# Kernel tuning notes

Measured on AMD Instinct MI355X. Metric: run time of the kernel, lower is better.

The kernel has to match this reference:

```python
import jax, jax.numpy as jnp
import numpy as np

N_NODES = 100000
N_EDGES = 1600000
D_IN = 128
HID = 128
E_CH = 16


def setup_inputs() -> dict:
    key = jax.random.key(0)
    ks = jax.random.split(key, 16)

    def glorot(k, shape):
        fan_in, fan_out = shape[0], shape[1]
        lim = jnp.sqrt(6.0 / (fan_in + fan_out))
        return jax.random.uniform(k, shape, jnp.float32, -lim, lim)

    inp = {
        "x": jax.random.normal(ks[0], (N_NODES, D_IN), jnp.float32),
        "edge_index": jax.random.randint(ks[1], (2, N_EDGES), 0, N_NODES, jnp.int32),
        "edge_attr": jax.random.normal(ks[2], (N_EDGES, E_CH), jnp.float32),
        # SAGEConv layer 0: lin_l (neighbor agg, with bias), lin_r (root, no bias)
        "Wl0": glorot(ks[3], (D_IN, HID)),
        "Wr0": glorot(ks[4], (D_IN, HID)),
        "b0": jnp.zeros((HID,), jnp.float32),
        # SAGEConv layer 1
        "Wl1": glorot(ks[5], (HID, HID)),
        "Wr1": glorot(ks[6], (HID, HID)),
        "b1": jnp.zeros((HID,), jnp.float32),
        # classifier MLP: (2*HID + E_CH) -> 128 -> 64 -> 1
        "Wc1": glorot(ks[7], (2 * HID + E_CH, 128)),
        "bc1": jnp.zeros((128,), jnp.float32),
        "Wc2": glorot(ks[8], (128, 64)),
        "bc2": jnp.zeros((64,), jnp.float32),
        "Wc3": glorot(ks[9], (64, 1)),
        "bc3": jnp.zeros((1,), jnp.float32),
    }
    return inp


def _sage_conv(x, src, dst, Wl, Wr, b):
    # PyG SAGEConv (aggr='mean'): out = lin_l(mean_j x_j) + lin_r(x_i)
    # messages flow src -> dst
    msg_sum = jax.ops.segment_sum(x[src], dst, num_segments=N_NODES)  # [N, D]
    deg = jax.ops.segment_sum(jnp.ones((src.shape[0],), x.dtype), dst,
                              num_segments=N_NODES)                   # [N]
    agg = msg_sum / jnp.maximum(deg, 1.0)[:, None]  # mean; isolated nodes -> 0
    return agg @ Wl + b + x @ Wr


def reference(x, edge_index, edge_attr,
              Wl0, Wr0, b0, Wl1, Wr1, b1,
              Wc1, bc1, Wc2, bc2, Wc3, bc3):
    src, dst = edge_index[0], edge_index[1]
    # encode: two SAGEConv layers, each followed by ReLU (dropout is identity at eval)
    h = jax.nn.relu(_sage_conv(x, src, dst, Wl0, Wr0, b0))
    h = jax.nn.relu(_sage_conv(h, src, dst, Wl1, Wr1, b1))
    # edge classifier: gather endpoint embeddings, concat edge features
    feat = jnp.concatenate([h[src], h[dst], edge_attr], axis=-1)  # [E, 2H+EC]
    z = jax.nn.relu(feat @ Wc1 + bc1)
    z = jax.nn.relu(z @ Wc2 + bc2)
    logits = (z @ Wc3 + bc3).reshape(-1)  # [E]
    return jax.nn.sigmoid(logits)
```

## Files before the change

kernel.cpp:

```cpp
#include <hip/hip_runtime.h>
#include <hip/hip_bf16.h>
#include <math.h>

#define NN 100000
#define NE 1600000
#define NBLK 391
#define ZS 296

typedef __bf16 bf16x8 __attribute__((ext_vector_type(8)));
typedef float f32x4 __attribute__((ext_vector_type(4)));

union BF8 { bf16x8 v; unsigned short u[8]; };

static __device__ __forceinline__ unsigned short f2bf(float f) {
  unsigned int u = __float_as_uint(f);
  unsigned int r = u + 0x7fffu + ((u >> 16) & 1u);
  return (unsigned short)(r >> 16);
}
static __device__ __forceinline__ float bf2f(unsigned short b) {
  return __uint_as_float((unsigned int)b << 16);
}
static __device__ __forceinline__ f32x4 zero4() {
  f32x4 z = {0.f, 0.f, 0.f, 0.f}; return z;
}
static __device__ __forceinline__ bf16x8 zerobf8() {
  BF8 t;
  #pragma unroll
  for (int j = 0; j < 8; ++j) t.u[j] = 0;
  return t.v;
}
static __device__ __forceinline__ bf16x8 cvt8(float4 v0, float4 v1, float s) {
  BF8 t;
  t.u[0]=f2bf(v0.x*s); t.u[1]=f2bf(v0.y*s); t.u[2]=f2bf(v0.z*s); t.u[3]=f2bf(v0.w*s);
  t.u[4]=f2bf(v1.x*s); t.u[5]=f2bf(v1.y*s); t.u[6]=f2bf(v1.z*s); t.u[7]=f2bf(v1.w*s);
  return t.v;
}

__global__ void prep_swizzle(const float* __restrict__ Wl0, const float* __restrict__ Wr0,
                             const float* __restrict__ Wl1, const float* __restrict__ Wr1,
                             const float* __restrict__ Wc1, const float* __restrict__ Wc2,
                             __hip_bfloat16* __restrict__ swz) {
  int gid = blockIdx.x * 256 + threadIdx.x;
  if (gid >= 110592) return;
  int id = gid;
  const float* A; const float* B = nullptr; int KC, Nc, Ksrc;
  if (id < 32768)        { KC = 8; Nc = 128; Ksrc = 256; A = Wl0; B = Wr0; }
  else if (id < 65536)   { id -= 32768; KC = 8; Nc = 128; Ksrc = 256; A = Wl1; B = Wr1; }
  else if (id < 81920)   { id -= 65536; KC = 4; Nc = 128; Ksrc = 128; A = Wc1; }
  else if (id < 98304)   { id -= 81920; KC = 4; Nc = 128; Ksrc = 128; A = Wc1 + 128 * 128; }
  else if (id < 102400)  { id -= 98304; KC = 1; Nc = 128; Ksrc = 16;  A = Wc1 + 256 * 128; }
  else                   { id -= 102400; KC = 4; Nc = 64;  Ksrc = 128; A = Wc2; }
  int j = id & 7, lane = (id >> 3) & 63, rest = id >> 9;
  int c = rest % KC, t = rest / KC;
  int k = c * 32 + (lane >> 4) * 8 + j;
  int n = t * 16 + (lane & 15);
  float v = 0.f;
  if (k < Ksrc) {
    if (B && k >= 128) v = B[(k - 128) * Nc + n];
    else               v = A[k * Nc + n];
  }
  unsigned short* o = (unsigned short*)swz;
  o[gid] = f2bf(v);
}

__global__ void x_to_bf16(const float* __restrict__ x, __hip_bfloat16* __restrict__ xb) {
  int i = blockIdx.x * 256 + threadIdx.x;
  float4 v = ((const float4*)x)[i];
  ushort4 p;
  p.x = f2bf(v.x); p.y = f2bf(v.y); p.z = f2bf(v.z); p.w = f2bf(v.w);
  ((ushort4*)xb)[i] = p;
}

__global__ void deg_count(const int* __restrict__ ei, int* __restrict__ degCnt) {
  int e = blockIdx.x * 256 + threadIdx.x;
  atomicAdd(&degCnt[ei[NE + e]], 1);
}

__global__ void scan_block_sums(const int* __restrict__ degCnt, int* __restrict__ blockSums) {
  __shared__ int red[4];
  int i = blockIdx.x * 256 + threadIdx.x;
  int v = (i < NN) ? degCnt[i] : 0;
  #pragma unroll
  for (int off = 32; off; off >>= 1) v += __shfl_down(v, off, 64);
  if ((threadIdx.x & 63) == 0) red[threadIdx.x >> 6] = v;
  __syncthreads();
  if (threadIdx.x == 0) blockSums[blockIdx.x] = red[0] + red[1] + red[2] + red[3];
}

__global__ void scan_partials(const int* __restrict__ blockSums, int* __restrict__ blockOff) {
  __shared__ int lds[512];
  int t = threadIdx.x;
  int v = (t < NBLK) ? blockSums[t] : 0;
  lds[t] = v; __syncthreads();
  #pragma unroll
  for (int off = 1; off < 512; off <<= 1) {
    int a = (t >= off) ? lds[t - off] : 0;
    __syncthreads();
    lds[t] += a;
    __syncthreads();
  }
  if (t < NBLK) blockOff[t] = lds[t] - v;
}

__global__ void scan_write(const int* __restrict__ degCnt, const int* __restrict__ blockOff,
                           int* __restrict__ rowPtr, int* __restrict__ cursor) {
  __shared__ int lds[256];
  int t = threadIdx.x;
  int i = blockIdx.x * 256 + t;
  int v = (i < NN) ? degCnt[i] : 0;
  lds[t] = v; __syncthreads();
  #pragma unroll
  for (int off = 1; off < 256; off <<= 1) {
    int a = (t >= off) ? lds[t - off] : 0;
    __syncthreads();
    lds[t] += a;
    __syncthreads();
  }
  if (i < NN) {
    int excl = blockOff[blockIdx.x] + lds[t] - v;
    rowPtr[i] = excl;
    cursor[i] = excl;
  }
}

__global__ void csr_fill(const int* __restrict__ ei, int* __restrict__ cursor,
                         int* __restrict__ csrSrc, int2* __restrict__ csrDE) {
  int e = blockIdx.x * 256 + threadIdx.x;
  int s = ei[e], d = ei[NE + e];
  int idx = atomicAdd(&cursor[d], 1);
  csrSrc[idx] = s;
  csrDE[idx] = make_int2(d, e);
}

__global__ __launch_bounds__(256, 8)
void gather_agg(const __hip_bfloat16* __restrict__ xb,
                const int* __restrict__ csrSrc, const int* __restrict__ rowPtr,
                const int* __restrict__ degCnt, __hip_bfloat16* __restrict__ msgOut) {
  int g = threadIdx.x >> 4, c16 = threadIdx.x & 15;
  int n = blockIdx.x * 16 + g;
  int rp = rowPtr[n], dg = degCnt[n];
  float a[8];
  #pragma unroll
  for (int j = 0; j < 8; ++j) a[j] = 0.f;
  for (int i = 0; i < dg; i += 4) {
    #pragma unroll
    for (int k = 0; k < 4; ++k) {
      int ii = i + k;
      int s = csrSrc[rp + (ii < dg ? ii : dg - 1)];
      uint4 u = *(const uint4*)((const unsigned short*)xb + (size_t)s * 128 + c16 * 8);
      if (ii < dg) {
        a[0] += bf2f((unsigned short)(u.x & 0xffff)); a[1] += bf2f((unsigned short)(u.x >> 16));
        a[2] += bf2f((unsigned short)(u.y & 0xffff)); a[3] += bf2f((unsigned short)(u.y >> 16));
        a[4] += bf2f((unsigned short)(u.z & 0xffff)); a[5] += bf2f((unsigned short)(u.z >> 16));
        a[6] += bf2f((unsigned short)(u.w & 0xffff)); a[7] += bf2f((unsigned short)(u.w >> 16));
      }
    }
  }
  float r = 1.f / fmaxf((float)dg, 1.f);
  uint4 p;
  p.x = (unsigned)f2bf(a[0] * r) | ((unsigned)f2bf(a[1] * r) << 16);
  p.y = (unsigned)f2bf(a[2] * r) | ((unsigned)f2bf(a[3] * r) << 16);
  p.z = (unsigned)f2bf(a[4] * r) | ((unsigned)f2bf(a[5] * r) << 16);
  p.w = (unsigned)f2bf(a[6] * r) | ((unsigned)f2bf(a[7] * r) << 16);
  *(uint4*)((unsigned short*)msgOut + (size_t)n * 128 + c16 * 8) = p;
}

__global__ __launch_bounds__(256, 2)
void node_gemm(const __hip_bfloat16* __restrict__ msgB,
               const __hip_bfloat16* __restrict__ selfB16,
               const __hip_bfloat16* __restrict__ swzW, const float* __restrict__ bias,
               __hip_bfloat16* __restrict__ hOut) {
  const int tid = threadIdx.x, w = tid >> 6, lane = tid & 63;
  const int l15 = lane & 15, quad = lane >> 4;
  const int nBase = blockIdx.x * 256 + w * 64;

  int row[4];
  #pragma unroll
  for (int t = 0; t < 4; ++t) {
    int n = nBase + t * 16 + l15;
    if (n > NN - 1) n = NN - 1;
    row[t] = n;
  }

  f32x4 acc[8][4];
  #pragma unroll
  for (int mt = 0; mt < 8; ++mt)
    #pragma unroll
    for (int nt = 0; nt < 4; ++nt) acc[mt][nt] = zero4();

  #pragma unroll
  for (int c = 0; c < 8; ++c) {
    bf16x8 bfr[4];
    if (c < 4) {
      #pragma unroll
      for (int nt = 0; nt < 4; ++nt)
        bfr[nt] = *(const bf16x8*)(msgB + (size_t)row[nt] * 128 + c * 32 + quad * 8);
    } else {
      #pragma unroll
      for (int nt = 0; nt < 4; ++nt)
        bfr[nt] = *(const bf16x8*)(selfB16 + (size_t)row[nt] * 128 + (c - 4) * 32 + quad * 8);
    }
    bf16x8 afr[8];
    #pragma unroll
    for (int mt = 0; mt < 8; ++mt)
      afr[mt] = *(const bf16x8*)(swzW + ((mt * 8 + c) * 64 + lane) * 8);
    #pragma unroll
    for (int mt = 0; mt < 8; ++mt)
      #pragma unroll
      for (int nt = 0; nt < 4; ++nt)
        acc[mt][nt] = __builtin_amdgcn_mfma_f32_16x16x32_bf16(afr[mt], bfr[nt], acc[mt][nt], 0, 0, 0);
  }

  #pragma unroll
  for (int mt = 0; mt < 8; ++mt) {
    const float4 b4 = *(const float4*)(bias + mt * 16 + quad * 4);
    #pragma unroll
    for (int nt = 0; nt < 4; ++nt) {
      int n = nBase + nt * 16 + l15;
      if (n < NN) {
        ushort4 p;
        p.x = f2bf(fmaxf(acc[mt][nt][0] + b4.x, 0.f));
        p.y = f2bf(fmaxf(acc[mt][nt][1] + b4.y, 0.f));
        p.z = f2bf(fmaxf(acc[mt][nt][2] + b4.z, 0.f));
        p.w = f2bf(fmaxf(acc[mt][nt][3] + b4.w, 0.f));
        *(ushort4*)(hOut + (size_t)n * 128 + mt * 16 + quad * 4) = p;
      }
    }
  }
}

__global__ __launch_bounds__(256, 2)
void pq_gemm(const __hip_bfloat16* __restrict__ h1, const __hip_bfloat16* __restrict__ swzPQ,
             __hip_bfloat16* __restrict__ Pout, __hip_bfloat16* __restrict__ Qout) {
  const __hip_bfloat16* swzW = swzPQ + blockIdx.y * 16384;
  __hip_bfloat16* outp = blockIdx.y ? Qout : Pout;
  const int tid = threadIdx.x, w = tid >> 6, lane = tid & 63;
  const int l15 = lane & 15, quad = lane >> 4;
  const int nBase = blockIdx.x * 256 + w * 64;

  int row[4];
  #pragma unroll
  for (int t = 0; t < 4; ++t) {
    int n = nBase + t * 16 + l15;
    if (n > NN - 1) n = NN - 1;
    row[t] = n;
  }

  f32x4 acc[8][4];
  #pragma unroll
  for (int mt = 0; mt < 8; ++mt)
    #pragma unroll
    for (int nt = 0; nt < 4; ++nt) acc[mt][nt] = zero4();

  #pragma unroll
  for (int c = 0; c < 4; ++c) {
    bf16x8 bfr[4];
    #pragma unroll
    for (int nt = 0; nt < 4; ++nt)
      bfr[nt] = *(const bf16x8*)(h1 + (size_t)row[nt] * 128 + c * 32 + quad * 8);
    bf16x8 afr[8];
    #pragma unroll
    for (int mt = 0; mt < 8; ++mt)
      afr[mt] = *(const bf16x8*)(swzW + ((mt * 4 + c) * 64 + lane) * 8);
    #pragma unroll
    for (int mt = 0; mt < 8; ++mt)
      #pragma unroll
      for (int nt = 0; nt < 4; ++nt)
        acc[mt][nt] = __builtin_amdgcn_mfma_f32_16x16x32_bf16(afr[mt], bfr[nt], acc[mt][nt], 0, 0, 0);
  }

  #pragma unroll
  for (int mt = 0; mt < 8; ++mt) {
    #pragma unroll
    for (int nt = 0; nt < 4; ++nt) {
      int n = nBase + nt * 16 + l15;
      if (n < NN) {
        ushort4 p;
        p.x = f2bf(acc[mt][nt][0]);
        p.y = f2bf(acc[mt][nt][1]);
        p.z = f2bf(acc[mt][nt][2]);
        p.w = f2bf(acc[mt][nt][3]);
        *(ushort4*)(outp + (size_t)n * 128 + mt * 16 + quad * 4) = p;
      }
    }
  }
}

__global__ __launch_bounds__(256, 4)
void edge_mlp(const __hip_bfloat16* __restrict__ P, const __hip_bfloat16* __restrict__ Q,
              const float* __restrict__ ea,
              const int* __restrict__ csrSrc, const int2* __restrict__ csrDE,
              const __hip_bfloat16* __restrict__ swzWea, const __hip_bfloat16* __restrict__ swzWc2,
              const float* __restrict__ Wc3, const float* __restrict__ bc1,
              const float* __restrict__ bc2, const float* __restrict__ bc3,
              float* __restrict__ out) {
  __shared__ char lds[4 * 32 * ZS];
  const int tid = threadIdx.x, w = tid >> 6, lane = tid & 63;
  const int l15 = lane & 15, quad = lane >> 4;
  const int eBase = blockIdx.x * 128 + w * 32;
  char* zbuf = lds + w * (32 * ZS);

  int srcO[2], dstO[2], eid[2];
  #pragma unroll
  for (int t = 0; t < 2; ++t) {
    int p = eBase + t * 16 + l15;
    srcO[t] = csrSrc[p] * 128;
    int2 de = csrDE[p];
    dstO[t] = de.x * 128;
    eid[t] = de.y;
  }

  ushort4 pA[2][4];
  #pragma unroll
  for (int nt = 0; nt < 2; ++nt)
    #pragma unroll
    for (int mt = 0; mt < 4; ++mt)
      pA[nt][mt] = *(const ushort4*)(P + srcO[nt] + mt * 16 + quad * 4);

  bf16x8 bfr[2];
  #pragma unroll
  for (int nt = 0; nt < 2; ++nt) {
    if (quad < 2) {
      const float4* pe = (const float4*)(ea + (size_t)eid[nt] * 16 + quad * 8);
      bfr[nt] = cvt8(pe[0], pe[1], 1.f);
    } else {
      bfr[nt] = zerobf8();
    }
  }

  f32x4 acc[4][2];
  #pragma unroll
  for (int mt = 0; mt < 4; ++mt)
    #pragma unroll
    for (int nt = 0; nt < 2; ++nt) acc[mt][nt] = zero4();
  #pragma unroll
  for (int mt = 0; mt < 4; ++mt) {
    bf16x8 afr = *(const bf16x8*)(swzWea + (mt * 64 + lane) * 8);
    #pragma unroll
    for (int nt = 0; nt < 2; ++nt)
      acc[mt][nt] = __builtin_amdgcn_mfma_f32_16x16x32_bf16(afr, bfr[nt], acc[mt][nt], 0, 0, 0);
  }

  ushort4 pB[2][4], qA[2][4];
  #pragma unroll
  for (int nt = 0; nt < 2; ++nt)
    #pragma unroll
    for (int mt = 0; mt < 4; ++mt)
      pB[nt][mt] = *(const ushort4*)(P + srcO[nt] + (mt + 4) * 16 + quad * 4);
  #pragma unroll
  for (int nt = 0; nt < 2; ++nt)
    #pragma unroll
    for (int mt = 0; mt < 4; ++mt)
      qA[nt][mt] = *(const ushort4*)(Q + dstO[nt] + mt * 16 + quad * 4);

  #pragma unroll
  for (int mt = 0; mt < 4; ++mt) {
    const int cb = mt * 16 + quad * 4;
    const float4 b4 = *(const float4*)(bc1 + cb);
    #pragma unroll
    for (int nt = 0; nt < 2; ++nt) {
      ushort4 pu = pA[nt][mt];
      ushort4 qu = qA[nt][mt];
      int er = nt * 16 + l15;
      ushort4 z;
      z.x = f2bf(fmaxf(acc[mt][nt][0] + bf2f(pu.x) + bf2f(qu.x) + b4.x, 0.f));
      z.y = f2bf(fmaxf(acc[mt][nt][1] + bf2f(pu.y) + bf2f(qu.y) + b4.y, 0.f));
      z.z = f2bf(fmaxf(acc[mt][nt][2] + bf2f(pu.z) + bf2f(qu.z) + b4.z, 0.f));
      z.w = f2bf(fmaxf(acc[mt][nt][3] + bf2f(pu.w) + bf2f(qu.w) + b4.w, 0.f));
      *(ushort4*)(zbuf + er * ZS + cb * 2) = z;
    }
  }

  #pragma unroll
  for (int mt = 0; mt < 4; ++mt)
    #pragma unroll
    for (int nt = 0; nt < 2; ++nt) acc[mt][nt] = zero4();
  #pragma unroll
  for (int mt = 0; mt < 4; ++mt) {
    bf16x8 afr = *(const bf16x8*)(swzWea + ((mt + 4) * 64 + lane) * 8);
    #pragma unroll
    for (int nt = 0; nt < 2; ++nt)
      acc[mt][nt] = __builtin_amdgcn_mfma_f32_16x16x32_bf16(afr, bfr[nt], acc[mt][nt], 0, 0, 0);
  }

  ushort4 qB[2][4];
  #pragma unroll
  for (int nt = 0; nt < 2; ++nt)
    #pragma unroll
    for (int mt = 0; mt < 4; ++mt)
      qB[nt][mt] = *(const ushort4*)(Q + dstO[nt] + (mt + 4) * 16 + quad * 4);

  #pragma unroll
  for (int mt = 0; mt < 4; ++mt) {
    const int cb = (mt + 4) * 16 + quad * 4;
    const float4 b4 = *(const float4*)(bc1 + cb);
    #pragma unroll
    for (int nt = 0; nt < 2; ++nt) {
      ushort4 pu = pB[nt][mt];
      ushort4 qu = qB[nt][mt];
      int er = nt * 16 + l15;
      ushort4 z;
      z.x = f2bf(fmaxf(acc[mt][nt][0] + bf2f(pu.x) + bf2f(qu.x) + b4.x, 0.f));
      z.y = f2bf(fmaxf(acc[mt][nt][1] + bf2f(pu.y) + bf2f(qu.y) + b4.y, 0.f));
      z.z = f2bf(fmaxf(acc[mt][nt][2] + bf2f(pu.z) + bf2f(qu.z) + b4.z, 0.f));
      z.w = f2bf(fmaxf(acc[mt][nt][3] + bf2f(pu.w) + bf2f(qu.w) + b4.w, 0.f));
      *(ushort4*)(zbuf + er * ZS + cb * 2) = z;
    }
  }

  f32x4 acc2[4][2];
  #pragma unroll
  for (int mt = 0; mt < 4; ++mt)
    #pragma unroll
    for (int nt = 0; nt < 2; ++nt) acc2[mt][nt] = zero4();

  #pragma unroll
  for (int c = 0; c < 4; ++c) {
    bf16x8 b2[2];
    #pragma unroll
    for (int nt = 0; nt < 2; ++nt)
      b2[nt] = *(const bf16x8*)(zbuf + (nt * 16 + l15) * ZS + (c * 32 + quad * 8) * 2);
    #pragma unroll
    for (int mt = 0; mt < 4; ++mt) {
      bf16x8 afr = *(const bf16x8*)(swzWc2 + ((mt * 4 + c) * 64 + lane) * 8);
      #pragma unroll
      for (int nt = 0; nt < 2; ++nt)
        acc2[mt][nt] = __builtin_amdgcn_mfma_f32_16x16x32_bf16(afr, b2[nt], acc2[mt][nt], 0, 0, 0);
    }
  }

  #pragma unroll
  for (int mt = 0; mt < 4; ++mt) {
    const int cb = mt * 16 + quad * 4;
    const float4 b4 = *(const float4*)(bc2 + cb);
    #pragma unroll
    for (int nt = 0; nt < 2; ++nt) {
      int er = nt * 16 + l15;
      ushort4 z;
      z.x = f2bf(fmaxf(acc2[mt][nt][0] + b4.x, 0.f));
      z.y = f2bf(fmaxf(acc2[mt][nt][1] + b4.y, 0.f));
      z.z = f2bf(fmaxf(acc2[mt][nt][2] + b4.z, 0.f));
      z.w = f2bf(fmaxf(acc2[mt][nt][3] + b4.w, 0.f));
      *(ushort4*)(zbuf + er * ZS + cb * 2) = z;
    }
  }

  {
    int e = lane & 31, half = lane >> 5;
    float a3 = (half == 0) ? bc3[0] : 0.f;
    #pragma unroll
    for (int k2 = 0; k2 < 16; ++k2) {
      unsigned int u = *(const unsigned int*)(zbuf + e * ZS + half * 64 + k2 * 4);
      float v0 = __uint_as_float(u << 16);
      float v1 = __uint_as_float(u & 0xffff0000u);
      const float2 wv = *(const float2*)(Wc3 + half * 32 + 2 * k2);
      a3 += v0 * wv.x + v1 * wv.y;
    }
    a3 += __shfl_xor(a3, 32);
    if (half == 0) {
      int oe = csrDE[eBase + e].y;
      out[oe] = 1.f / (1.f + __expf(-a3));
    }
  }
}

extern "C" void kernel_launch(void* const* d_in, const int* in_sizes, int n_in,
                              void* d_out, int out_size, void* d_ws, size_t ws_size,
                              hipStream_t stream) {
  const float* x   = (const float*)d_in[0];
  const int*   ei  = (const int*)d_in[1];
  const float* ea  = (const float*)d_in[2];
  const float* Wl0 = (const float*)d_in[3];
  const float* Wr0 = (const float*)d_in[4];
  const float* b0  = (const float*)d_in[5];
  const float* Wl1 = (const float*)d_in[6];
  const float* Wr1 = (const float*)d_in[7];
  const float* b1  = (const float*)d_in[8];
  const float* Wc1 = (const float*)d_in[9];
  const float* bc1 = (const float*)d_in[10];
  const float* Wc2 = (const float*)d_in[11];
  const float* bc2 = (const float*)d_in[12];
  const float* Wc3 = (const float*)d_in[13];
  const float* bc3 = (const float*)d_in[14];
  float* out = (float*)d_out;

  char* ws = (char*)d_ws;
  int* degCnt    = (int*)(ws + 0);
  int* rowPtr    = (int*)(ws + 400000);
  int* cursor    = (int*)(ws + 800000);
  int* blockSums = (int*)(ws + 1200000);
  int* blockOff  = (int*)(ws + 1202048);
  int* csrSrc    = (int*)(ws + 1204096);
  int2* csrDE    = (int2*)(ws + 7604096);
  __hip_bfloat16* bufB = (__hip_bfloat16*)(ws + 20404096);
  __hip_bfloat16* bufC = (__hip_bfloat16*)(ws + 46004096);
  __hip_bfloat16* bufD = (__hip_bfloat16*)(ws + 71604096);
  __hip_bfloat16* swz  = (__hip_bfloat16*)(ws + 97204096);
  __hip_bfloat16* msgB = bufB; __hip_bfloat16* Pb = bufB;
  __hip_bfloat16* h0b  = bufC; __hip_bfloat16* Qb = bufC;
  __hip_bfloat16* xb   = bufD; __hip_bfloat16* h1b = bufD;

  hipMemsetAsync(degCnt, 0, 400000, stream);
  prep_swizzle<<<432, 256, 0, stream>>>(Wl0, Wr0, Wl1, Wr1, Wc1, Wc2, swz);
  x_to_bf16<<<12500, 256, 0, stream>>>(x, xb);

  deg_count<<<NE / 256, 256, 0, stream>>>(ei, degCnt);
  scan_block_sums<<<NBLK, 256, 0, stream>>>(degCnt, blockSums);
  scan_partials<<<1, 512, 0, stream>>>(blockSums, blockOff);
  scan_write<<<NBLK, 256, 0, stream>>>(degCnt, blockOff, rowPtr, cursor);
  csr_fill<<<NE / 256, 256, 0, stream>>>(ei, cursor, csrSrc, csrDE);

  gather_agg<<<NN / 16, 256, 0, stream>>>(xb, csrSrc, rowPtr, degCnt, msgB);
  node_gemm<<<NBLK, 256, 0, stream>>>(msgB, xb, swz, b0, h0b);

  gather_agg<<<NN / 16, 256, 0, stream>>>(h0b, csrSrc, rowPtr, degCnt, msgB);
  node_gemm<<<NBLK, 256, 0, stream>>>(msgB, h0b, swz + 32768, b1, h1b);

  pq_gemm<<<dim3(NBLK, 2), 256, 0, stream>>>(h1b, swz + 65536, Pb, Qb);
  edge_mlp<<<NE / 128, 256, 0, stream>>>(Pb, Qb, ea, csrSrc, csrDE,
                                         swz + 98304, swz + 102400,
                                         Wc3, bc1, bc2, bc3, out);
}
```

Baseline: 845.9 us.

## Fuse neighbor gather, SAGE node GEMM and P/Q projection into one kernel

Replaces the separate gather_agg, node_gemm and pq_gemm launches with a single fused_sage kernel per layer. Each block aggregates 64 nodes into LDS, then runs the node GEMM from LDS; on the second layer h1 stays in LDS and feeds the P/Q projection directly. This removes the global round trips for the mean-aggregated messages and for h1, plus three launches. In exchange each block handles fewer nodes, the weight fragments are re-read by many more blocks, and occupancy is tied to the 34 KB of LDS per block.

```diff
diff --git a/kernel.cpp b/kernel.cpp
--- a/kernel.cpp
+++ b/kernel.cpp
@@ -6,6 +6,7 @@
 #define NE 1600000
 #define NBLK 391
 #define ZS 296
+#define RS 272
 
 typedef __bf16 bf16x8 __attribute__((ext_vector_type(8)));
 typedef float f32x4 __attribute__((ext_vector_type(4)));
@@ -132,155 +133,159 @@
   csrDE[idx] = make_int2(d, e);
 }
 
-__global__ __launch_bounds__(256, 8)
-void gather_agg(const __hip_bfloat16* __restrict__ xb,
+__global__ __launch_bounds__(256, 4)
+void fused_sage(const __hip_bfloat16* __restrict__ feat,
                 const int* __restrict__ csrSrc, const int* __restrict__ rowPtr,
-                const int* __restrict__ degCnt, __hip_bfloat16* __restrict__ msgOut) {
-  int g = threadIdx.x >> 4, c16 = threadIdx.x & 15;
-  int n = blockIdx.x * 16 + g;
-  int rp = rowPtr[n], dg = degCnt[n];
-  float a[8];
-  #pragma unroll
-  for (int j = 0; j < 8; ++j) a[j] = 0.f;
-  for (int i = 0; i < dg; i += 4) {
-    #pragma unroll
-    for (int k = 0; k < 4; ++k) {
-      int ii = i + k;
-      int s = csrSrc[rp + (ii < dg ? ii : dg - 1)];
-      uint4 u = *(const uint4*)((const unsigned short*)xb + (size_t)s * 128 + c16 * 8);
-      if (ii < dg) {
-        a[0] += bf2f((unsigned short)(u.x & 0xffff)); a[1] += bf2f((unsigned short)(u.x >> 16));
-        a[2] += bf2f((unsigned short)(u.y & 0xffff)); a[3] += bf2f((unsigned short)(u.y >> 16));
-        a[4] += bf2f((unsigned short)(u.z & 0xffff)); a[5] += bf2f((unsigned short)(u.z >> 16));
-        a[6] += bf2f((unsigned short)(u.w & 0xffff)); a[7] += bf2f((unsigned short)(u.w >> 16));
+                const int* __restrict__ degCnt,
+                const __hip_bfloat16* __restrict__ swzW, const float* __restrict__ bias,
+                __hip_bfloat16* __restrict__ hOut,
+                int doPQ, const __hip_bfloat16* __restrict__ swzPQ,
+                __hip_bfloat16* __restrict__ Pout, __hip_bfloat16* __restrict__ Qout) {
+  __shared__ __align__(16) char msgL[64 * RS];
+  __shared__ __align__(16) char hL[64 * RS];
+  const int tid = threadIdx.x;
+  const int nBase = blockIdx.x * 64;
+
+  {
+    int g = tid >> 4, c16 = tid & 15;
+    for (int r = 0; r < 4; ++r) {
+      int nl = r * 16 + g;
+      int n = nBase + nl;
+      float a[8];
+      #pragma unroll
+      for (int j = 0; j < 8; ++j) a[j] = 0.f;
+      float rinv = 0.f;
+      if (n < NN) {
+        int rp = rowPtr[n], dg = degCnt[n];
+        for (int i = 0; i < dg; i += 4) {
+          #pragma unroll
+          for (int k = 0; k < 4; ++k) {
+            int ii = i + k;
+            int s = csrSrc[rp + (ii < dg ? ii : dg - 1)];
+            uint4 u = *(const uint4*)((const unsigned short*)feat + (size_t)s * 128 + c16 * 8);
+            if (ii < dg) {
+              a[0] += bf2f((unsigned short)(u.x & 0xffff)); a[1] += bf2f((unsigned short)(u.x >> 16));
+              a[2] += bf2f((unsigned short)(u.y & 0xffff)); a[3] += bf2f((unsigned short)(u.y >> 16));
+              a[4] += bf2f((unsigned short)(u.z & 0xffff)); a[5] += bf2f((unsigned short)(u.z >> 16));
+              a[6] += bf2f((unsigned short)(u.w & 0xffff)); a[7] += bf2f((unsigned short)(u.w >> 16));
+            }
+          }
+        }
+        rinv = 1.f / fmaxf((float)dg, 1.f);
       }
-    }
-  }
-  float r = 1.f / fmaxf((float)dg, 1.f);
-  uint4 p;
-  p.x = (unsigned)f2bf(a[0] * r) | ((unsigned)f2bf(a[1] * r) << 16);
-  p.y = (unsigned)f2bf(a[2] * r) | ((unsigned)f2bf(a[3] * r) << 16);
-  p.z = (unsigned)f2bf(a[4] * r) | ((unsigned)f2bf(a[5] * r) << 16);
-  p.w = (unsigned)f2bf(a[6] * r) | ((unsigned)f2bf(a[7] * r) << 16);
-  *(uint4*)((unsigned short*)msgOut + (size_t)n * 128 + c16 * 8) = p;
-}
-
-__global__ __launch_bounds__(256, 2)
-void node_gemm(const __hip_bfloat16* __restrict__ msgB,
-               const __hip_bfloat16* __restrict__ selfB16,
-               const __hip_bfloat16* __restrict__ swzW, const float* __restrict__ bias,
-               __hip_bfloat16* __restrict__ hOut) {
-  const int tid = threadIdx.x, w = tid >> 6, lane = tid & 63;
+      uint4 p;
+      p.x = (unsigned)f2bf(a[0] * rinv) | ((unsigned)f2bf(a[1] * rinv) << 16);
+      p.y = (unsigned)f2bf(a[2] * rinv) | ((unsigned)f2bf(a[3] * rinv) << 16);
+      p.z = (unsigned)f2bf(a[4] * rinv) | ((unsigned)f2bf(a[5] * rinv) << 16);
+      p.w = (unsigned)f2bf(a[6] * rinv) | ((unsigned)f2bf(a[7] * rinv) << 16);
+      *(uint4*)(msgL + nl * RS + c16 * 16) = p;
+    }
+  }
+  __syncthreads();
+
+  const int w = tid >> 6, lane = tid & 63;
   const int l15 = lane & 15, quad = lane >> 4;
-  const int nBase = blockIdx.x * 256 + w * 64;
-
-  int row[4];
-  #pragma unroll
-  for (int t = 0; t < 4; ++t) {
-    int n = nBase + t * 16 + l15;
-    if (n > NN - 1) n = NN - 1;
-    row[t] = n;
-  }
-
-  f32x4 acc[8][4];
-  #pragma unroll
-  for (int mt = 0; mt < 8; ++mt)
-    #pragma unroll
-    for (int nt = 0; nt < 4; ++nt) acc[mt][nt] = zero4();
-
-  #pragma unroll
-  for (int c = 0; c < 8; ++c) {
-    bf16x8 bfr[4];
-    if (c < 4) {
+  int rowg[4];
+  #pragma unroll
+  for (int nt = 0; nt < 4; ++nt) {
+    int n = nBase + nt * 16 + l15;
+    rowg[nt] = (n < NN) ? n : (NN - 1);
+  }
+
+  {
+    f32x4 acc[2][4];
+    #pragma unroll
+    for (int mi = 0; mi < 2; ++mi)
+      #pragma unroll
+      for (int nt = 0; nt < 4; ++nt) acc[mi][nt] = zero4();
+
+    #pragma unroll
+    for (int c = 0; c < 8; ++c) {
+      bf16x8 bfr[4];
+      if (c < 4) {
+        #pragma unroll
+        for (int nt = 0; nt < 4; ++nt)
+          bfr[nt] = *(const bf16x8*)(msgL + (nt * 16 + l15) * RS + (c * 32 + quad * 8) * 2);
+      } else {
+        #pragma unroll
+        for (int nt = 0; nt < 4; ++nt)
+          bfr[nt] = *(const bf16x8*)(feat + (size_t)rowg[nt] * 128 + (c - 4) * 32 + quad * 8);
+      }
+      #pragma unroll
+      for (int mi = 0; mi < 2; ++mi) {
+        int mt = w * 2 + mi;
+        bf16x8 afr = *(const bf16x8*)(swzW + ((mt * 8 + c) * 64 + lane) * 8);
+        #pragma unroll
+        for (int nt = 0; nt < 4; ++nt)
+          acc[mi][nt] = __builtin_amdgcn_mfma_f32_16x16x32_bf16(afr, bfr[nt], acc[mi][nt], 0, 0, 0);
+      }
+    }
+
+    #pragma unroll
+    for (int mi = 0; mi < 2; ++mi) {
+      int mt = w * 2 + mi;
+      const int cb = mt * 16 + quad * 4;
+      const float4 b4 = *(const float4*)(bias + cb);
+      #pragma unroll
+      for (int nt = 0; nt < 4; ++nt) {
+        ushort4 p;
+        p.x = f2bf(fmaxf(acc[mi][nt][0] + b4.x, 0.f));
+        p.y = f2bf(fmaxf(acc[mi][nt][1] + b4.y, 0.f));
+        p.z = f2bf(fmaxf(acc[mi][nt][2] + b4.z, 0.f));
+        p.w = f2bf(fmaxf(acc[mi][nt][3] + b4.w, 0.f));
+        if (doPQ) {
+          *(ushort4*)(hL + (nt * 16 + l15) * RS + cb * 2) = p;
+        } else {
+          int n = nBase + nt * 16 + l15;
+          if (n < NN)
+            *(ushort4*)(hOut + (size_t)n * 128 + cb) = p;
+        }
+      }
+    }
+  }
+
+  if (doPQ) {
+    __syncthreads();
+    f32x4 acc2[4][4];
+    #pragma unroll
+    for (int mi = 0; mi < 4; ++mi)
+      #pragma unroll
+      for (int nt = 0; nt < 4; ++nt) acc2[mi][nt] = zero4();
+
+    #pragma unroll
+    for (int c = 0; c < 4; ++c) {
+      bf16x8 bfr[4];
       #pragma unroll
       for (int nt = 0; nt < 4; ++nt)
-        bfr[nt] = *(const bf16x8*)(msgB + (size_t)row[nt] * 128 + c * 32 + quad * 8);
-    } else {
-      #pragma unroll
-      for (int nt = 0; nt < 4; ++nt)
-        bfr[nt] = *(const bf16x8*)(selfB16 + (size_t)row[nt] * 128 + (c - 4) * 32 + quad * 8);
-    }
-    bf16x8 afr[8];
-    #pragma unroll
-    for (int mt = 0; mt < 8; ++mt)
-      afr[mt] = *(const bf16x8*)(swzW + ((mt * 8 + c) * 64 + lane) * 8);
-    #pragma unroll
-    for (int mt = 0; mt < 8; ++mt)
-      #pragma unroll
-      for (int nt = 0; nt < 4; ++nt)
-        acc[mt][nt] = __builtin_amdgcn_mfma_f32_16x16x32_bf16(afr[mt], bfr[nt], acc[mt][nt], 0, 0, 0);
-  }
-
-  #pragma unroll
-  for (int mt = 0; mt < 8; ++mt) {
-    const float4 b4 = *(const float4*)(bias + mt * 16 + quad * 4);
-    #pragma unroll
-    for (int nt = 0; nt < 4; ++nt) {
-      int n = nBase + nt * 16 + l15;
-      if (n < NN) {
-        ushort4 p;
-        p.x = f2bf(fmaxf(acc[mt][nt][0] + b4.x, 0.f));
-        p.y = f2bf(fmaxf(acc[mt][nt][1] + b4.y, 0.f));
-        p.z = f2bf(fmaxf(acc[mt][nt][2] + b4.z, 0.f));
-        p.w = f2bf(fmaxf(acc[mt][nt][3] + b4.w, 0.f));
-        *(ushort4*)(hOut + (size_t)n * 128 + mt * 16 + quad * 4) = p;
+        bfr[nt] = *(const bf16x8*)(hL + (nt * 16 + l15) * RS + (c * 32 + quad * 8) * 2);
+      #pragma unroll
+      for (int mi = 0; mi < 4; ++mi) {
+        int mtg = w * 4 + mi;
+        const __hip_bfloat16* base = swzPQ + ((mtg < 8) ? 0 : 16384);
+        int t = mtg & 7;
+        bf16x8 afr = *(const bf16x8*)(base + ((t * 4 + c) * 64 + lane) * 8);
+        #pragma unroll
+        for (int nt = 0; nt < 4; ++nt)
+          acc2[mi][nt] = __builtin_amdgcn_mfma_f32_16x16x32_bf16(afr, bfr[nt], acc2[mi][nt], 0, 0, 0);
       }
     }
-  }
-}
-
-__global__ __launch_bounds__(256, 2)
-void pq_gemm(const __hip_bfloat16* __restrict__ h1, const __hip_bfloat16* __restrict__ swzPQ,
-             __hip_bfloat16* __restrict__ Pout, __hip_bfloat16* __restrict__ Qout) {
-  const __hip_bfloat16* swzW = swzPQ + blockIdx.y * 16384;
-  __hip_bfloat16* outp = blockIdx.y ? Qout : Pout;
-  const int tid = threadIdx.x, w = tid >> 6, lane = tid & 63;
-  const int l15 = lane & 15, quad = lane >> 4;
-  const int nBase = blockIdx.x * 256 + w * 64;
-
-  int row[4];
-  #pragma unroll
-  for (int t = 0; t < 4; ++t) {
-    int n = nBase + t * 16 + l15;
-    if (n > NN - 1) n = NN - 1;
-    row[t] = n;
-  }
-
-  f32x4 acc[8][4];
-  #pragma unroll
-  for (int mt = 0; mt < 8; ++mt)
-    #pragma unroll
-    for (int nt = 0; nt < 4; ++nt) acc[mt][nt] = zero4();
-
-  #pragma unroll
-  for (int c = 0; c < 4; ++c) {
-    bf16x8 bfr[4];
-    #pragma unroll
-    for (int nt = 0; nt < 4; ++nt)
-      bfr[nt] = *(const bf16x8*)(h1 + (size_t)row[nt] * 128 + c * 32 + quad * 8);
-    bf16x8 afr[8];
-    #pragma unroll
-    for (int mt = 0; mt < 8; ++mt)
-      afr[mt] = *(const bf16x8*)(swzW + ((mt * 4 + c) * 64 + lane) * 8);
-    #pragma unroll
-    for (int mt = 0; mt < 8; ++mt)
-      #pragma unroll
-      for (int nt = 0; nt < 4; ++nt)
-        acc[mt][nt] = __builtin_amdgcn_mfma_f32_16x16x32_bf16(afr[mt], bfr[nt], acc[mt][nt], 0, 0, 0);
-  }
-
-  #pragma unroll
-  for (int mt = 0; mt < 8; ++mt) {
-    #pragma unroll
-    for (int nt = 0; nt < 4; ++nt) {
-      int n = nBase + nt * 16 + l15;
-      if (n < NN) {
-        ushort4 p;
-        p.x = f2bf(acc[mt][nt][0]);
-        p.y = f2bf(acc[mt][nt][1]);
-        p.z = f2bf(acc[mt][nt][2]);
-        p.w = f2bf(acc[mt][nt][3]);
-        *(ushort4*)(outp + (size_t)n * 128 + mt * 16 + quad * 4) = p;
+
+    #pragma unroll
+    for (int mi = 0; mi < 4; ++mi) {
+      int mtg = w * 4 + mi;
+      __hip_bfloat16* outp = (mtg < 8) ? Pout : Qout;
+      const int cb = (mtg & 7) * 16 + quad * 4;
+      #pragma unroll
+      for (int nt = 0; nt < 4; ++nt) {
+        int n = nBase + nt * 16 + l15;
+        if (n < NN) {
+          ushort4 p;
+          p.x = f2bf(acc2[mi][nt][0]);
+          p.y = f2bf(acc2[mi][nt][1]);
+          p.z = f2bf(acc2[mi][nt][2]);
+          p.w = f2bf(acc2[mi][nt][3]);
+          *(ushort4*)(outp + (size_t)n * 128 + cb) = p;
+        }
       }
     }
   }
@@ -496,9 +501,10 @@
   __hip_bfloat16* bufC = (__hip_bfloat16*)(ws + 46004096);
   __hip_bfloat16* bufD = (__hip_bfloat16*)(ws + 71604096);
   __hip_bfloat16* swz  = (__hip_bfloat16*)(ws + 97204096);
-  __hip_bfloat16* msgB = bufB; __hip_bfloat16* Pb = bufB;
-  __hip_bfloat16* h0b  = bufC; __hip_bfloat16* Qb = bufC;
-  __hip_bfloat16* xb   = bufD; __hip_bfloat16* h1b = bufD;
+  __hip_bfloat16* Pb  = bufB;
+  __hip_bfloat16* h0b = bufC;
+  __hip_bfloat16* xb  = bufD;
+  __hip_bfloat16* Qb  = bufD;
 
   hipMemsetAsync(degCnt, 0, 400000, stream);
   prep_swizzle<<<432, 256, 0, stream>>>(Wl0, Wr0, Wl1, Wr1, Wc1, Wc2, swz);
@@ -510,13 +516,11 @@
   scan_write<<<NBLK, 256, 0, stream>>>(degCnt, blockOff, rowPtr, cursor);
   csr_fill<<<NE / 256, 256, 0, stream>>>(ei, cursor, csrSrc, csrDE);
 
-  gather_agg<<<NN / 16, 256, 0, stream>>>(xb, csrSrc, rowPtr, degCnt, msgB);
-  node_gemm<<<NBLK, 256, 0, stream>>>(msgB, xb, swz, b0, h0b);
-
-  gather_agg<<<NN / 16, 256, 0, stream>>>(h0b, csrSrc, rowPtr, degCnt, msgB);
-  node_gemm<<<NBLK, 256, 0, stream>>>(msgB, h0b, swz + 32768, b1, h1b);
-
-  pq_gemm<<<dim3(NBLK, 2), 256, 0, stream>>>(h1b, swz + 65536, Pb, Qb);
+  fused_sage<<<1563, 256, 0, stream>>>(xb, csrSrc, rowPtr, degCnt, swz, b0, h0b,
+                                       0, nullptr, nullptr, nullptr);
+  fused_sage<<<1563, 256, 0, stream>>>(h0b, csrSrc, rowPtr, degCnt, swz + 32768, b1, nullptr,
+                                       1, swz + 65536, Pb, Qb);
+
   edge_mlp<<<NE / 128, 256, 0, stream>>>(Pb, Qb, ea, csrSrc, csrDE,
                                          swz + 98304, swz + 102400,
                                          Wc3, bc1, bc2, bc3, out);
```

New measurement: 897.2 us. 6.1% more time.

## Fuse layer-1 SAGE GEMM with P/Q projection via LDS-resident h1

Applied to the files above, without the earlier changes.

The second node_gemm and the pq_gemm kernel are merged into one kernel. Each warp writes its bias+ReLU h1 tile to LDS and immediately runs both P and Q projections from it. This removes the global write and re-read of h1 and one kernel launch. In exchange, each block uses about 75 KB of LDS, the P/Q work runs on half as many blocks, and buffers are re-aliased so P overwrites msgB in place.

```diff
diff --git a/kernel.cpp b/kernel.cpp
--- a/kernel.cpp
+++ b/kernel.cpp
@@ -230,13 +230,16 @@
 }
 
 __global__ __launch_bounds__(256, 2)
-void pq_gemm(const __hip_bfloat16* __restrict__ h1, const __hip_bfloat16* __restrict__ swzPQ,
-             __hip_bfloat16* __restrict__ Pout, __hip_bfloat16* __restrict__ Qout) {
-  const __hip_bfloat16* swzW = swzPQ + blockIdx.y * 16384;
-  __hip_bfloat16* outp = blockIdx.y ? Qout : Pout;
+void node_pq_gemm(const __hip_bfloat16* __restrict__ msgB,
+                  const __hip_bfloat16* __restrict__ selfB16,
+                  const __hip_bfloat16* __restrict__ swzW, const float* __restrict__ bias,
+                  const __hip_bfloat16* __restrict__ swzPQ,
+                  __hip_bfloat16* __restrict__ Pout, __hip_bfloat16* __restrict__ Qout) {
+  __shared__ __align__(16) char hLds[4 * 64 * ZS];
   const int tid = threadIdx.x, w = tid >> 6, lane = tid & 63;
   const int l15 = lane & 15, quad = lane >> 4;
   const int nBase = blockIdx.x * 256 + w * 64;
+  char* hbuf = hLds + w * (64 * ZS);
 
   int row[4];
   #pragma unroll
@@ -246,41 +249,91 @@
     row[t] = n;
   }
 
-  f32x4 acc[8][4];
-  #pragma unroll
-  for (int mt = 0; mt < 8; ++mt)
-    #pragma unroll
-    for (int nt = 0; nt < 4; ++nt) acc[mt][nt] = zero4();
-
-  #pragma unroll
-  for (int c = 0; c < 4; ++c) {
-    bf16x8 bfr[4];
-    #pragma unroll
-    for (int nt = 0; nt < 4; ++nt)
-      bfr[nt] = *(const bf16x8*)(h1 + (size_t)row[nt] * 128 + c * 32 + quad * 8);
-    bf16x8 afr[8];
+  {
+    f32x4 acc[8][4];
     #pragma unroll
     for (int mt = 0; mt < 8; ++mt)
-      afr[mt] = *(const bf16x8*)(swzW + ((mt * 4 + c) * 64 + lane) * 8);
+      #pragma unroll
+      for (int nt = 0; nt < 4; ++nt) acc[mt][nt] = zero4();
+
+    #pragma unroll
+    for (int c = 0; c < 8; ++c) {
+      bf16x8 bfr[4];
+      if (c < 4) {
+        #pragma unroll
+        for (int nt = 0; nt < 4; ++nt)
+          bfr[nt] = *(const bf16x8*)(msgB + (size_t)row[nt] * 128 + c * 32 + quad * 8);
+      } else {
+        #pragma unroll
+        for (int nt = 0; nt < 4; ++nt)
+          bfr[nt] = *(const bf16x8*)(selfB16 + (size_t)row[nt] * 128 + (c - 4) * 32 + quad * 8);
+      }
+      bf16x8 afr[8];
+      #pragma unroll
+      for (int mt = 0; mt < 8; ++mt)
+        afr[mt] = *(const bf16x8*)(swzW + ((mt * 8 + c) * 64 + lane) * 8);
+      #pragma unroll
+      for (int mt = 0; mt < 8; ++mt)
+        #pragma unroll
+        for (int nt = 0; nt < 4; ++nt)
+          acc[mt][nt] = __builtin_amdgcn_mfma_f32_16x16x32_bf16(afr[mt], bfr[nt], acc[mt][nt], 0, 0, 0);
+    }
+
+    #pragma unroll
+    for (int mt = 0; mt < 8; ++mt) {
+      const int cb = mt * 16 + quad * 4;
+      const float4 b4 = *(const float4*)(bias + cb);
+      #pragma unroll
+      for (int nt = 0; nt < 4; ++nt) {
+        ushort4 p;
+        p.x = f2bf(fmaxf(acc[mt][nt][0] + b4.x, 0.f));
+        p.y = f2bf(fmaxf(acc[mt][nt][1] + b4.y, 0.f));
+        p.z = f2bf(fmaxf(acc[mt][nt][2] + b4.z, 0.f));
+        p.w = f2bf(fmaxf(acc[mt][nt][3] + b4.w, 0.f));
+        *(ushort4*)(hbuf + (nt * 16 + l15) * ZS + cb * 2) = p;
+      }
+    }
+  }
+
+  for (int hf = 0; hf < 2; ++hf) {
+    const __hip_bfloat16* swzH = swzPQ + hf * 16384;
+    __hip_bfloat16* outp = hf ? Qout : Pout;
+    f32x4 acc2[8][4];
     #pragma unroll
     for (int mt = 0; mt < 8; ++mt)
       #pragma unroll
+      for (int nt = 0; nt < 4; ++nt) acc2[mt][nt] = zero4();
+
+    #pragma unroll
+    for (int c = 0; c < 4; ++c) {
+      bf16x8 bfr[4];
+      #pragma unroll
       for (int nt = 0; nt < 4; ++nt)
-        acc[mt][nt] = __builtin_amdgcn_mfma_f32_16x16x32_bf16(afr[mt], bfr[nt], acc[mt][nt], 0, 0, 0);
-  }
-
-  #pragma unroll
-  for (int mt = 0; mt < 8; ++mt) {
-    #pragma unroll
-    for (int nt = 0; nt < 4; ++nt) {
-      int n = nBase + nt * 16 + l15;
-      if (n < NN) {
-        ushort4 p;
-        p.x = f2bf(acc[mt][nt][0]);
-        p.y = f2bf(acc[mt][nt][1]);
-        p.z = f2bf(acc[mt][nt][2]);
-        p.w = f2bf(acc[mt][nt][3]);
-        *(ushort4*)(outp + (size_t)n * 128 + mt * 16 + quad * 4) = p;
+        bfr[nt] = *(const bf16x8*)(hbuf + (nt * 16 + l15) * ZS + (c * 32 + quad * 8) * 2);
+      bf16x8 afr[8];
+      #pragma unroll
+      for (int mt = 0; mt < 8; ++mt)
+        afr[mt] = *(const bf16x8*)(swzH + ((mt * 4 + c) * 64 + lane) * 8);
+      #pragma unroll
+      for (int mt = 0; mt < 8; ++mt)
+        #pragma unroll
+        for (int nt = 0; nt < 4; ++nt)
+          acc2[mt][nt] = __builtin_amdgcn_mfma_f32_16x16x32_bf16(afr[mt], bfr[nt], acc2[mt][nt], 0, 0, 0);
+    }
+
+    #pragma unroll
+    for (int mt = 0; mt < 8; ++mt) {
+      #pragma unroll
+      for (int nt = 0; nt < 4; ++nt) {
+        int n = nBase + nt * 16 + l15;
+        if (n < NN) {
+          ushort4 p;
+          p.x = f2bf(acc2[mt][nt][0]);
+          p.y = f2bf(acc2[mt][nt][1]);
+          p.z = f2bf(acc2[mt][nt][2]);
+          p.w = f2bf(acc2[mt][nt][3]);
+          *(ushort4*)(outp + (size_t)n * 128 + mt * 16 + quad * 4) = p;
+        }
       }
     }
   }
@@ -497,8 +550,8 @@
   __hip_bfloat16* bufD = (__hip_bfloat16*)(ws + 71604096);
   __hip_bfloat16* swz  = (__hip_bfloat16*)(ws + 97204096);
   __hip_bfloat16* msgB = bufB; __hip_bfloat16* Pb = bufB;
-  __hip_bfloat16* h0b  = bufC; __hip_bfloat16* Qb = bufC;
-  __hip_bfloat16* xb   = bufD; __hip_bfloat16* h1b = bufD;
+  __hip_bfloat16* h0b  = bufC;
+  __hip_bfloat16* xb   = bufD; __hip_bfloat16* Qb = bufD;
 
   hipMemsetAsync(degCnt, 0, 400000, stream);
   prep_swizzle<<<432, 256, 0, stream>>>(Wl0, Wr0, Wl1, Wr1, Wc1, Wc2, swz);
@@ -514,9 +567,9 @@
   node_gemm<<<NBLK, 256, 0, stream>>>(msgB, xb, swz, b0, h0b);
 
   gather_agg<<<NN / 16, 256, 0, stream>>>(h0b, csrSrc, rowPtr, degCnt, msgB);
-  node_gemm<<<NBLK, 256, 0, stream>>>(msgB, h0b, swz + 32768, b1, h1b);
-
-  pq_gemm<<<dim3(NBLK, 2), 256, 0, stream>>>(h1b, swz + 65536, Pb, Qb);
+  node_pq_gemm<<<NBLK, 256, 0, stream>>>(msgB, h0b, swz + 32768, b1,
+                                         swz + 65536, Pb, Qb);
+
   edge_mlp<<<NE / 128, 256, 0, stream>>>(Pb, Qb, ea, csrSrc, csrDE,
                                          swz + 98304, swz + 102400,
                                          Wc3, bc1, bc2, bc3, out);
```

New measurement: 842.4 us. About the same (-0.4%).
